# Optimization experiments

Hardware: AMD Instinct MI355X
Metric: run time of the kernel (lower is better)

Reference implementation:

```python
import jax, jax.numpy as jnp
import numpy as np

B, T, N, H = 256, 128, 512, 128  # batch, timesteps, input_size (driving series), hidden


def setup_inputs() -> dict:
    key = jax.random.key(0)
    ks = jax.random.split(key, 7)
    p = lambda k, shape: (jax.random.normal(k, shape, dtype=jnp.float32) * 0.05)
    return {
        "X": jax.random.normal(ks[0], (B, T, N), dtype=jnp.float32),
        # attention linear: in_features = 2H + T, out_features = 1 (stored as a vector + scalar bias)
        "attn_w": p(ks[1], (2 * H + T,)),
        "attn_b": p(ks[2], ()),
        # LSTM cell params, PyTorch layout/gate order (i, f, g, o)
        "w_ih": p(ks[3], (4 * H, N)),
        "w_hh": p(ks[4], (4 * H, H)),
        "b_ih": p(ks[5], (4 * H,)),
        "b_hh": p(ks[6], (4 * H,)),
    }


def reference(X, attn_w, attn_b, w_ih, w_hh, b_ih, b_hh):
    Bn, Tn, Nn = X.shape
    Hh = w_hh.shape[1]
    # split the single attention weight row into the h / s / X-row pieces of the concat
    w_h, w_s, w_x = attn_w[:Hh], attn_w[Hh:2 * Hh], attn_w[2 * Hh:]
    Xp = jnp.swapaxes(X, 1, 2)            # [B, N, T]  (X.permute(0,2,1))
    x_score = Xp @ w_x                    # [B, N], time-invariant part of attention logits

    def step(carry, x_t):                 # x_t: [B, N] = X[:, t, :]
        h, c = carry
        # logits[b,i] = w_h.h[b] + w_s.c[b] + w_x.Xp[b,i] + b  (== Linear on the concat)
        score = x_score + (h @ w_h + c @ w_s + attn_b)[:, None]   # [B, N]
        alpha = jax.nn.softmax(score, axis=1)
        x_tilde = alpha * x_t                                      # [B, N]
        gates = x_tilde @ w_ih.T + h @ w_hh.T + b_ih + b_hh        # [B, 4H]
        i, f, g, o = jnp.split(gates, 4, axis=1)
        c_new = jax.nn.sigmoid(f) * c + jax.nn.sigmoid(i) * jnp.tanh(g)
        h_new = jax.nn.sigmoid(o) * jnp.tanh(c_new)
        return (h_new, c_new), (x_tilde, h_new)

    h0 = jnp.zeros((Bn, Hh), X.dtype)
    (_, _), (Xt, Xe) = jax.lax.scan(step, (h0, h0), jnp.swapaxes(X, 0, 1))
    # scan stacks along time -> [T, B, .]; return [B, T, .]
    return jnp.swapaxes(Xt, 0, 1), jnp.swapaxes(Xe, 0, 1)
```

## Files before the change

### kernel.cpp

```cpp
#include <hip/hip_runtime.h>
#include <hip/hip_bf16.h>

#define Bb 256
#define Tt 128
#define Nn 512
#define Hh 128

typedef __attribute__((ext_vector_type(4))) float floatx4;
typedef __attribute__((ext_vector_type(8))) short short8;
typedef _Float16 h2v_t __attribute__((ext_vector_type(2)));

__device__ __forceinline__ unsigned short f2bf(float f) {
  unsigned u = __float_as_uint(f);
  u += 0x7fffu + ((u >> 16) & 1u);
  return (unsigned short)(u >> 16);
}

__device__ __forceinline__ float sigmoid_fast(float x) {
  return __builtin_amdgcn_rcpf(1.f + __expf(-x));
}
__device__ __forceinline__ float tanh_fast(float x) {
  float e = __expf(2.f * x);
  return 1.f - 2.f * __builtin_amdgcn_rcpf(e + 1.f);
}

__device__ __forceinline__ void lds_barrier() {
  asm volatile("s_waitcnt lgkmcnt(0)" ::: "memory");
  __builtin_amdgcn_s_barrier();
  asm volatile("" ::: "memory");
}

__device__ __forceinline__ void async_load16(const void* g, void* lds) {
  __builtin_amdgcn_global_load_lds(
      (const __attribute__((address_space(1))) unsigned int*)g,
      (__attribute__((address_space(3))) unsigned int*)lds, 16, 0, 0);
}

#if __has_builtin(__builtin_amdgcn_fdot2)
#define FDOT2(a, b, c) __builtin_amdgcn_fdot2((a), (b), (c), false)
#else
__device__ __forceinline__ float fdot2_sw(h2v_t a, h2v_t b, float c) {
  return fmaf((float)a.x, (float)b.x, fmaf((float)a.y, (float)b.y, (c)));
}
#define FDOT2(a, b, c) fdot2_sw((a), (b), (c))
#endif

template <int CTRL>
__device__ __forceinline__ float qbcast(float x) {
#if __has_builtin(__builtin_amdgcn_update_dpp)
  return __uint_as_float((unsigned)__builtin_amdgcn_update_dpp(
      0, (int)__float_as_uint(x), CTRL, 0xf, 0xf, true));
#else
  return __shfl(x, (threadIdx.x & ~3) + (CTRL & 3), 64);
#endif
}

__global__ void prep_kernel(const float* __restrict__ w_ih,
                            const float* __restrict__ b_ih,
                            const float* __restrict__ b_hh,
                            unsigned short* __restrict__ wb,
                            float* __restrict__ bias) {
  int i = blockIdx.x * 256 + threadIdx.x;
  if (i < 4 * Hh * Nn) wb[i] = f2bf(w_ih[i]);
  if (i < 4 * Hh) bias[i] = b_ih[i] + b_hh[i];
}

__global__ __launch_bounds__(512) void alpha_kernel(const float* __restrict__ X,
                                                    const float* __restrict__ attn_w,
                                                    float* __restrict__ alpha) {
  int b = blockIdx.x;
  int tid = threadIdx.x;
  int c = tid & 127;
  int tp = tid >> 7;
  const float4* Xb = (const float4*)(X + (size_t)b * Tt * Nn) + c;
  const float* wx = attn_w + 2 * Hh;

  float4 acc = {0.f, 0.f, 0.f, 0.f};
#pragma unroll 8
  for (int tt = 0; tt < 32; ++tt) {
    int t = tp * 32 + tt;
    float4 x = Xb[(size_t)t * 128];
    float w = wx[t];
    acc.x = fmaf(x.x, w, acc.x);
    acc.y = fmaf(x.y, w, acc.y);
    acc.z = fmaf(x.z, w, acc.z);
    acc.w = fmaf(x.w, w, acc.w);
  }

  __shared__ float4 s4[512];
  __shared__ float sred[128];
  s4[tid] = acc;
  __syncthreads();

  float4 sc = {0.f, 0.f, 0.f, 0.f};
  if (tid < 128) {
    float4 a = s4[tid], b2 = s4[tid + 128], c2 = s4[tid + 256], d = s4[tid + 384];
    sc.x = a.x + b2.x + c2.x + d.x;
    sc.y = a.y + b2.y + c2.y + d.y;
    sc.z = a.z + b2.z + c2.z + d.z;
    sc.w = a.w + b2.w + c2.w + d.w;
    sred[tid] = fmaxf(fmaxf(sc.x, sc.y), fmaxf(sc.z, sc.w));
  }
  __syncthreads();
  for (int s = 64; s > 0; s >>= 1) {
    if (tid < s) sred[tid] = fmaxf(sred[tid], sred[tid + s]);
    __syncthreads();
  }
  float m = sred[0];
  __syncthreads();

  float4 e4 = {0.f, 0.f, 0.f, 0.f};
  if (tid < 128) {
    e4.x = __expf(sc.x - m);
    e4.y = __expf(sc.y - m);
    e4.z = __expf(sc.z - m);
    e4.w = __expf(sc.w - m);
    sred[tid] = e4.x + e4.y + e4.z + e4.w;
  }
  __syncthreads();
  for (int s = 64; s > 0; s >>= 1) {
    if (tid < s) sred[tid] += sred[tid + s];
    __syncthreads();
  }
  float inv = 1.f / sred[0];
  if (tid < 128) {
    float4 out;
    out.x = e4.x * inv; out.y = e4.y * inv; out.z = e4.z * inv; out.w = e4.w * inv;
    ((float4*)(alpha + (size_t)b * Nn))[tid] = out;
  }
}

__global__ __launch_bounds__(256) void scale_kernel(const float* __restrict__ X,
                                                    const float* __restrict__ alpha,
                                                    float* __restrict__ Xt,
                                                    unsigned short* __restrict__ xtb) {
  size_t i = (size_t)blockIdx.x * 256 + threadIdx.x;
  size_t e = i * 4;
  int n = (int)(e & (Nn - 1));
  int brow = (int)(e >> 9);
  int b = brow >> 7;
  float4 x = ((const float4*)X)[i];
  float4 a = *(const float4*)(alpha + (size_t)b * Nn + n);
  float4 y;
  y.x = x.x * a.x; y.y = x.y * a.y; y.z = x.z * a.z; y.w = x.w * a.w;
  ((float4*)Xt)[i] = y;
  ushort4 u;
  u.x = f2bf(y.x); u.y = f2bf(y.y); u.z = f2bf(y.z); u.w = f2bf(y.w);
  ((ushort4*)xtb)[i] = u;
}

#define GBK 64

__global__ __launch_bounds__(256) void gemm_bt(const unsigned short* __restrict__ A,
                                               const unsigned short* __restrict__ Bw,
                                               const float* __restrict__ bias,
                                               float* __restrict__ C) {
  __shared__ __align__(16) unsigned short As[128 * 64];
  __shared__ __align__(16) unsigned short Bs[128 * 64];
  const int K = 512, NO = 512;
  int tid = threadIdx.x;
  int lane = tid & 63;
  int wave = tid >> 6;
  int wm = wave & 1, wn = wave >> 1;
  int l15 = lane & 15;
  int quad = lane >> 4;
  int mtile = blockIdx.x, ntile = blockIdx.y;

  floatx4 acc[4][4];
#pragma unroll
  for (int i = 0; i < 4; ++i)
#pragma unroll
    for (int j = 0; j < 4; ++j) acc[i][j] = (floatx4){0.f, 0.f, 0.f, 0.f};

  int lr = lane >> 3;
  int lc = (lane & 7) ^ lr;
  const size_t lane_goff = (size_t)lr * K + lc * 8;
  const size_t abase = (size_t)mtile * 128 * K + lane_goff;
  const size_t bbase = (size_t)ntile * 128 * K + lane_goff;
  int sw = (quad ^ (l15 & 7)) * 8;

  for (int kb = 0; kb < K; kb += GBK) {
#pragma unroll
    for (int slot = 0; slot < 4; ++slot) {
      int r0 = slot * 32 + wave * 8;
      async_load16(A + abase + (size_t)r0 * K + kb, &As[r0 * 64]);
      async_load16(Bw + bbase + (size_t)r0 * K + kb, &Bs[r0 * 64]);
    }
    __syncthreads();
#pragma unroll
    for (int kh = 0; kh < 2; ++kh) {
      int sc = sw ^ (kh * 32);
      short8 af[4], bf[4];
#pragma unroll
      for (int i = 0; i < 4; ++i)
        af[i] = *(const short8*)(&As[(wm * 64 + i * 16 + l15) * 64 + sc]);
#pragma unroll
      for (int j = 0; j < 4; ++j)
        bf[j] = *(const short8*)(&Bs[(wn * 64 + j * 16 + l15) * 64 + sc]);
#pragma unroll
      for (int i = 0; i < 4; ++i)
#pragma unroll
        for (int j = 0; j < 4; ++j)
          acc[i][j] = __builtin_amdgcn_mfma_f32_16x16x32_bf16(af[i], bf[j], acc[i][j], 0, 0, 0);
    }
    __syncthreads();
  }

  int m0 = mtile * 128 + wm * 64;
  int n0 = ntile * 128 + wn * 64;
#pragma unroll
  for (int j = 0; j < 4; ++j) {
    int col = n0 + j * 16 + l15;
    float bsum = bias[col];
#pragma unroll
    for (int i = 0; i < 4; ++i) {
      int row = m0 + i * 16 + quad * 4;
#pragma unroll
      for (int r = 0; r < 4; ++r)
        C[(size_t)(row + r) * NO + col] = acc[i][j][r] + bsum;
    }
  }
}

__global__ __launch_bounds__(512, 1) void lstm_kernel(const float* __restrict__ G,
                                                      const float* __restrict__ w_hh,
                                                      float* __restrict__ Xe) {
  int b = blockIdx.x;
  int tid = threadIdx.x;
  int u = tid >> 2;
  int f = tid & 3;

  h2v_t wreg[64];
  {
    const float4* wr = (const float4*)(w_hh + (size_t)(f * 128 + u) * 128);
#pragma unroll
    for (int i = 0; i < 32; ++i) {
      float4 v = wr[i];
      wreg[2 * i]     = (h2v_t){(_Float16)v.x, (_Float16)v.y};
      wreg[2 * i + 1] = (h2v_t){(_Float16)v.z, (_Float16)v.w};
    }
  }

  __shared__ __align__(16) unsigned short h2[2][128];
  if (tid < 128) h2[0][tid] = 0;
  __syncthreads();

  const float* Gb = G + (size_t)b * Tt * 512 + f * 128 + u;
  float* Xeb = Xe + (size_t)b * Tt * Hh;

  float gcur = Gb[0];
  float gnext = Gb[512];
  float c0 = 0.f;

  const float actm = (f == 2) ? 2.f : -1.f;
  const float fA   = (f == 2) ? -2.f : 1.f;
  const float fB   = (f == 2) ? 1.f : 0.f;

#define H2F(W) __builtin_bit_cast(h2v_t, (W))

  for (int t = 0; t < Tt; ++t) {
    int cur = t & 1;
    const uint4* hp = (const uint4*)(&h2[cur][0]);

    float g_this = gcur;
    gcur = gnext;
    if (t + 2 < Tt) gnext = Gb[(size_t)(t + 2) * 512];

    float a0 = g_this, a1 = 0.f;
#pragma unroll
    for (int ch = 0; ch < 4; ++ch) {
      uint4 r0 = hp[ch * 4 + 0], r1 = hp[ch * 4 + 1];
      uint4 r2 = hp[ch * 4 + 2], r3 = hp[ch * 4 + 3];
      const h2v_t* wk = &wreg[ch * 16];
      a0 = FDOT2(H2F(r0.x), wk[0],  a0);  a1 = FDOT2(H2F(r0.y), wk[1],  a1);
      a0 = FDOT2(H2F(r0.z), wk[2],  a0);  a1 = FDOT2(H2F(r0.w), wk[3],  a1);
      a0 = FDOT2(H2F(r1.x), wk[4],  a0);  a1 = FDOT2(H2F(r1.y), wk[5],  a1);
      a0 = FDOT2(H2F(r1.z), wk[6],  a0);  a1 = FDOT2(H2F(r1.w), wk[7],  a1);
      a0 = FDOT2(H2F(r2.x), wk[8],  a0);  a1 = FDOT2(H2F(r2.y), wk[9],  a1);
      a0 = FDOT2(H2F(r2.z), wk[10], a0);  a1 = FDOT2(H2F(r2.w), wk[11], a1);
      a0 = FDOT2(H2F(r3.x), wk[12], a0);  a1 = FDOT2(H2F(r3.y), wk[13], a1);
      a0 = FDOT2(H2F(r3.z), wk[14], a0);  a1 = FDOT2(H2F(r3.w), wk[15], a1);
    }
    float x = a0 + a1;

    float e = __expf(x * actm);
    float r = __builtin_amdgcn_rcpf(1.f + e);
    float val = fmaf(r, fA, fB);

    float gi = qbcast<0x00>(val);
    float gf = qbcast<0x55>(val);
    float gg = qbcast<0xAA>(val);
    float go = qbcast<0xFF>(val);

    c0 = fmaf(gf, c0, gi * gg);
    float hv = go * tanh_fast(c0);

    if (f == 0) h2[cur ^ 1][u] = __builtin_bit_cast(unsigned short, (_Float16)hv);
    if (f == 1) Xeb[(size_t)t * Hh + u] = hv;
    lds_barrier();
  }
#undef H2F
}

extern "C" void kernel_launch(void* const* d_in, const int* in_sizes, int n_in,
                              void* d_out, int out_size, void* d_ws, size_t ws_size,
                              hipStream_t stream) {
  const float* X      = (const float*)d_in[0];
  const float* attn_w = (const float*)d_in[1];
  const float* w_ih   = (const float*)d_in[3];
  const float* w_hh   = (const float*)d_in[4];
  const float* b_ih   = (const float*)d_in[5];
  const float* b_hh   = (const float*)d_in[6];

  float* Xt = (float*)d_out;
  float* Xe = (float*)d_out + (size_t)Bb * Tt * Nn;

  char* ws = (char*)d_ws;
  float*          alpha = (float*)(ws);
  float*          bias  = (float*)(ws + 524288);
  unsigned short* wb    = (unsigned short*)(ws + 526336);
  unsigned short* xtb   = (unsigned short*)(ws + 1050624);
  float*          G     = (float*)(ws + 34605056);

  prep_kernel<<<dim3(1024), dim3(256), 0, stream>>>(w_ih, b_ih, b_hh, wb, bias);
  alpha_kernel<<<dim3(Bb), dim3(512), 0, stream>>>(X, attn_w, alpha);
  scale_kernel<<<dim3(16384), dim3(256), 0, stream>>>(X, alpha, Xt, xtb);
  gemm_bt<<<dim3(256, 4), dim3(256), 0, stream>>>(xtb, wb, bias, G);
  lstm_kernel<<<dim3(Bb), dim3(512), 0, stream>>>(G, w_hh, Xe);
}
```

Measured before the change: 276.6 us.

## Batch LSTM recurrence onto MFMA over 16 rows and fuse alpha with scaling

The LSTM recurrence now processes 16 batch rows per block. The h·W_hh product runs as bf16 MFMA 16x16x32, with W_hh held in registers as B fragments and h kept in swizzled LDS. This replaces the per-row fp16 dot2 path and cuts the block count from 256 to 16. Separately, the alpha softmax and the X scaling/bf16 conversion are fused into one kernel, dropping the alpha round trip and one launch. Only 16 blocks on a large GPU means low occupancy for the serial recurrence, and bf16 for h/W_hh lowers precision compared with fp16.

```diff
diff --git a/kernel.cpp b/kernel.cpp
--- a/kernel.cpp
+++ b/kernel.cpp
@@ -8,7 +8,6 @@
 
 typedef __attribute__((ext_vector_type(4))) float floatx4;
 typedef __attribute__((ext_vector_type(8))) short short8;
-typedef _Float16 h2v_t __attribute__((ext_vector_type(2)));
 
 __device__ __forceinline__ unsigned short f2bf(float f) {
   unsigned u = __float_as_uint(f);
@@ -34,25 +33,6 @@
   __builtin_amdgcn_global_load_lds(
       (const __attribute__((address_space(1))) unsigned int*)g,
       (__attribute__((address_space(3))) unsigned int*)lds, 16, 0, 0);
-}
-
-#if __has_builtin(__builtin_amdgcn_fdot2)
-#define FDOT2(a, b, c) __builtin_amdgcn_fdot2((a), (b), (c), false)
-#else
-__device__ __forceinline__ float fdot2_sw(h2v_t a, h2v_t b, float c) {
-  return fmaf((float)a.x, (float)b.x, fmaf((float)a.y, (float)b.y, (c)));
-}
-#define FDOT2(a, b, c) fdot2_sw((a), (b), (c))
-#endif
-
-template <int CTRL>
-__device__ __forceinline__ float qbcast(float x) {
-#if __has_builtin(__builtin_amdgcn_update_dpp)
-  return __uint_as_float((unsigned)__builtin_amdgcn_update_dpp(
-      0, (int)__float_as_uint(x), CTRL, 0xf, 0xf, true));
-#else
-  return __shfl(x, (threadIdx.x & ~3) + (CTRL & 3), 64);
-#endif
 }
 
 __global__ void prep_kernel(const float* __restrict__ w_ih,
@@ -65,21 +45,22 @@
   if (i < 4 * Hh) bias[i] = b_ih[i] + b_hh[i];
 }
 
-__global__ __launch_bounds__(512) void alpha_kernel(const float* __restrict__ X,
-                                                    const float* __restrict__ attn_w,
-                                                    float* __restrict__ alpha) {
+__global__ __launch_bounds__(512) void alpha_scale_kernel(const float* __restrict__ X,
+                                                          const float* __restrict__ attn_w,
+                                                          float* __restrict__ Xt,
+                                                          unsigned short* __restrict__ xtb) {
   int b = blockIdx.x;
   int tid = threadIdx.x;
   int c = tid & 127;
   int tp = tid >> 7;
-  const float4* Xb = (const float4*)(X + (size_t)b * Tt * Nn) + c;
+  const float4* Xb4 = (const float4*)(X + (size_t)b * Tt * Nn);
   const float* wx = attn_w + 2 * Hh;
 
   float4 acc = {0.f, 0.f, 0.f, 0.f};
 #pragma unroll 8
   for (int tt = 0; tt < 32; ++tt) {
     int t = tp * 32 + tt;
-    float4 x = Xb[(size_t)t * 128];
+    float4 x = Xb4[(size_t)t * 128 + c];
     float w = wx[t];
     acc.x = fmaf(x.x, w, acc.x);
     acc.y = fmaf(x.y, w, acc.y);
@@ -89,6 +70,7 @@
 
   __shared__ float4 s4[512];
   __shared__ float sred[128];
+  __shared__ __align__(16) float salpha[512];
   s4[tid] = acc;
   __syncthreads();
 
@@ -126,27 +108,25 @@
   if (tid < 128) {
     float4 out;
     out.x = e4.x * inv; out.y = e4.y * inv; out.z = e4.z * inv; out.w = e4.w * inv;
-    ((float4*)(alpha + (size_t)b * Nn))[tid] = out;
-  }
-}
-
-__global__ __launch_bounds__(256) void scale_kernel(const float* __restrict__ X,
-                                                    const float* __restrict__ alpha,
-                                                    float* __restrict__ Xt,
-                                                    unsigned short* __restrict__ xtb) {
-  size_t i = (size_t)blockIdx.x * 256 + threadIdx.x;
-  size_t e = i * 4;
-  int n = (int)(e & (Nn - 1));
-  int brow = (int)(e >> 9);
-  int b = brow >> 7;
-  float4 x = ((const float4*)X)[i];
-  float4 a = *(const float4*)(alpha + (size_t)b * Nn + n);
-  float4 y;
-  y.x = x.x * a.x; y.y = x.y * a.y; y.z = x.z * a.z; y.w = x.w * a.w;
-  ((float4*)Xt)[i] = y;
-  ushort4 u;
-  u.x = f2bf(y.x); u.y = f2bf(y.y); u.z = f2bf(y.z); u.w = f2bf(y.w);
-  ((ushort4*)xtb)[i] = u;
+    ((float4*)salpha)[tid] = out;
+  }
+  __syncthreads();
+
+  float4* Xt4 = (float4*)(Xt + (size_t)b * Tt * Nn);
+  ushort4* xt4 = (ushort4*)(xtb + (size_t)b * Tt * Nn);
+#pragma unroll 4
+  for (int i = 0; i < 32; ++i) {
+    int idx = i * 512 + tid;
+    int n4 = idx & 127;
+    float4 x = Xb4[idx];
+    float4 a = *(const float4*)(&salpha[n4 * 4]);
+    float4 y;
+    y.x = x.x * a.x; y.y = x.y * a.y; y.z = x.z * a.z; y.w = x.w * a.w;
+    Xt4[idx] = y;
+    ushort4 u;
+    u.x = f2bf(y.x); u.y = f2bf(y.y); u.z = f2bf(y.z); u.w = f2bf(y.w);
+    xt4[idx] = u;
+  }
 }
 
 #define GBK 64
@@ -225,81 +205,103 @@
 __global__ __launch_bounds__(512, 1) void lstm_kernel(const float* __restrict__ G,
                                                       const float* __restrict__ w_hh,
                                                       float* __restrict__ Xe) {
-  int b = blockIdx.x;
+  int b0 = blockIdx.x * 16;
   int tid = threadIdx.x;
-  int u = tid >> 2;
-  int f = tid & 3;
-
-  h2v_t wreg[64];
+  int wn = tid >> 6;
+  int lane = tid & 63;
+  int l15 = lane & 15;
+  int quad = lane >> 4;
+
+  short8 bfr[4][4];
+#pragma unroll
+  for (int j = 0; j < 4; ++j) {
+    const float* src = w_hh + (size_t)(j * 128 + wn * 16 + l15) * 128;
+#pragma unroll
+    for (int kf = 0; kf < 4; ++kf) {
+      int k0 = kf * 32 + quad * 8;
+      float4 lo = *(const float4*)(src + k0);
+      float4 hi = *(const float4*)(src + k0 + 4);
+      short8 v;
+      v[0] = (short)f2bf(lo.x); v[1] = (short)f2bf(lo.y);
+      v[2] = (short)f2bf(lo.z); v[3] = (short)f2bf(lo.w);
+      v[4] = (short)f2bf(hi.x); v[5] = (short)f2bf(hi.y);
+      v[6] = (short)f2bf(hi.z); v[7] = (short)f2bf(hi.w);
+      bfr[j][kf] = v;
+    }
+  }
+
+  __shared__ __align__(16) unsigned short h2[2][16 * 128];
   {
-    const float4* wr = (const float4*)(w_hh + (size_t)(f * 128 + u) * 128);
-#pragma unroll
-    for (int i = 0; i < 32; ++i) {
-      float4 v = wr[i];
-      wreg[2 * i]     = (h2v_t){(_Float16)v.x, (_Float16)v.y};
-      wreg[2 * i + 1] = (h2v_t){(_Float16)v.z, (_Float16)v.w};
-    }
-  }
-
-  __shared__ __align__(16) unsigned short h2[2][128];
-  if (tid < 128) h2[0][tid] = 0;
-  __syncthreads();
-
-  const float* Gb = G + (size_t)b * Tt * 512 + f * 128 + u;
-  float* Xeb = Xe + (size_t)b * Tt * Hh;
-
-  float gcur = Gb[0];
-  float gnext = Gb[512];
-  float c0 = 0.f;
-
-  const float actm = (f == 2) ? 2.f : -1.f;
-  const float fA   = (f == 2) ? -2.f : 1.f;
-  const float fB   = (f == 2) ? 1.f : 0.f;
-
-#define H2F(W) __builtin_bit_cast(h2v_t, (W))
+    uint4 z;
+    z.x = 0u; z.y = 0u; z.z = 0u; z.w = 0u;
+    ((uint4*)h2)[tid] = z;
+  }
+  __syncthreads();
+
+  const float* Gr[4];
+#pragma unroll
+  for (int r = 0; r < 4; ++r)
+    Gr[r] = G + ((size_t)(b0 + quad * 4 + r) * Tt) * 512 + wn * 16 + l15;
+
+  float gcur[4][4], gnext[4][4];
+#pragma unroll
+  for (int j = 0; j < 4; ++j)
+#pragma unroll
+    for (int r = 0; r < 4; ++r) {
+      gcur[j][r] = Gr[r][0 * 512 + j * 128];
+      gnext[j][r] = Gr[r][1 * 512 + j * 128];
+    }
+
+  float c0[4] = {0.f, 0.f, 0.f, 0.f};
+  float* Xeb = Xe + (size_t)wn * 16 + l15;
+  int swz = (l15 & 7) << 4;
 
   for (int t = 0; t < Tt; ++t) {
     int cur = t & 1;
-    const uint4* hp = (const uint4*)(&h2[cur][0]);
-
-    float g_this = gcur;
-    gcur = gnext;
-    if (t + 2 < Tt) gnext = Gb[(size_t)(t + 2) * 512];
-
-    float a0 = g_this, a1 = 0.f;
-#pragma unroll
-    for (int ch = 0; ch < 4; ++ch) {
-      uint4 r0 = hp[ch * 4 + 0], r1 = hp[ch * 4 + 1];
-      uint4 r2 = hp[ch * 4 + 2], r3 = hp[ch * 4 + 3];
-      const h2v_t* wk = &wreg[ch * 16];
-      a0 = FDOT2(H2F(r0.x), wk[0],  a0);  a1 = FDOT2(H2F(r0.y), wk[1],  a1);
-      a0 = FDOT2(H2F(r0.z), wk[2],  a0);  a1 = FDOT2(H2F(r0.w), wk[3],  a1);
-      a0 = FDOT2(H2F(r1.x), wk[4],  a0);  a1 = FDOT2(H2F(r1.y), wk[5],  a1);
-      a0 = FDOT2(H2F(r1.z), wk[6],  a0);  a1 = FDOT2(H2F(r1.w), wk[7],  a1);
-      a0 = FDOT2(H2F(r2.x), wk[8],  a0);  a1 = FDOT2(H2F(r2.y), wk[9],  a1);
-      a0 = FDOT2(H2F(r2.z), wk[10], a0);  a1 = FDOT2(H2F(r2.w), wk[11], a1);
-      a0 = FDOT2(H2F(r3.x), wk[12], a0);  a1 = FDOT2(H2F(r3.y), wk[13], a1);
-      a0 = FDOT2(H2F(r3.z), wk[14], a0);  a1 = FDOT2(H2F(r3.w), wk[15], a1);
-    }
-    float x = a0 + a1;
-
-    float e = __expf(x * actm);
-    float r = __builtin_amdgcn_rcpf(1.f + e);
-    float val = fmaf(r, fA, fB);
-
-    float gi = qbcast<0x00>(val);
-    float gf = qbcast<0x55>(val);
-    float gg = qbcast<0xAA>(val);
-    float go = qbcast<0xFF>(val);
-
-    c0 = fmaf(gf, c0, gi * gg);
-    float hv = go * tanh_fast(c0);
-
-    if (f == 0) h2[cur ^ 1][u] = __builtin_bit_cast(unsigned short, (_Float16)hv);
-    if (f == 1) Xeb[(size_t)t * Hh + u] = hv;
+    const char* hbase = (const char*)&h2[cur][0] + l15 * 256;
+    short8 af[4];
+#pragma unroll
+    for (int kf = 0; kf < 4; ++kf)
+      af[kf] = *(const short8*)(hbase + ((kf * 64 + quad * 16) ^ swz));
+
+    floatx4 acc[4];
+#pragma unroll
+    for (int j = 0; j < 4; ++j)
+      acc[j] = (floatx4){gcur[j][0], gcur[j][1], gcur[j][2], gcur[j][3]};
+#pragma unroll
+    for (int j = 0; j < 4; ++j)
+#pragma unroll
+      for (int r = 0; r < 4; ++r) gcur[j][r] = gnext[j][r];
+    if (t + 2 < Tt) {
+#pragma unroll
+      for (int r = 0; r < 4; ++r)
+#pragma unroll
+        for (int j = 0; j < 4; ++j)
+          gnext[j][r] = Gr[r][(size_t)(t + 2) * 512 + j * 128];
+    }
+
+#pragma unroll
+    for (int kf = 0; kf < 4; ++kf)
+#pragma unroll
+      for (int j = 0; j < 4; ++j)
+        acc[j] = __builtin_amdgcn_mfma_f32_16x16x32_bf16(af[kf], bfr[j][kf], acc[j], 0, 0, 0);
+
+    unsigned short* hw = &h2[cur ^ 1][0];
+#pragma unroll
+    for (int r = 0; r < 4; ++r) {
+      float si = sigmoid_fast(acc[0][r]);
+      float sf = sigmoid_fast(acc[1][r]);
+      float tg = tanh_fast(acc[2][r]);
+      float so = sigmoid_fast(acc[3][r]);
+      c0[r] = fmaf(sf, c0[r], si * tg);
+      float hv = so * tanh_fast(c0[r]);
+      int row = quad * 4 + r;
+      int cb = (2 * (wn * 16 + l15)) ^ ((row & 7) << 4);
+      *(unsigned short*)((char*)hw + row * 256 + cb) = f2bf(hv);
+      Xeb[((size_t)(b0 + row) * Tt + t) * Hh] = hv;
+    }
     lds_barrier();
   }
-#undef H2F
 }
 
 extern "C" void kernel_launch(void* const* d_in, const int* in_sizes, int n_in,
@@ -316,15 +318,13 @@
   float* Xe = (float*)d_out + (size_t)Bb * Tt * Nn;
 
   char* ws = (char*)d_ws;
-  float*          alpha = (float*)(ws);
   float*          bias  = (float*)(ws + 524288);
   unsigned short* wb    = (unsigned short*)(ws + 526336);
   unsigned short* xtb   = (unsigned short*)(ws + 1050624);
   float*          G     = (float*)(ws + 34605056);
 
   prep_kernel<<<dim3(1024), dim3(256), 0, stream>>>(w_ih, b_ih, b_hh, wb, bias);
-  alpha_kernel<<<dim3(Bb), dim3(512), 0, stream>>>(X, attn_w, alpha);
-  scale_kernel<<<dim3(16384), dim3(256), 0, stream>>>(X, alpha, Xt, xtb);
+  alpha_scale_kernel<<<dim3(Bb), dim3(512), 0, stream>>>(X, attn_w, Xt, xtb);
   gemm_bt<<<dim3(256, 4), dim3(256), 0, stream>>>(xtb, wb, bias, G);
-  lstm_kernel<<<dim3(Bb), dim3(512), 0, stream>>>(G, w_hh, Xe);
-}
+  lstm_kernel<<<dim3(Bb / 16), dim3(512), 0, stream>>>(G, w_hh, Xe);
+}
```

New measurement: 380.1 us. 1.37x slower.
